# Kernel optimization log

Measured on AMD Instinct MI355X. Metric: run time of the kernel, lower is better.

The kernel has to match this reference:

```python
import jax, jax.numpy as jnp
import numpy as np

DIM = 192
NUM_HEADS = 6
KSZ = 7
MLP_RATIO = 4.0
LEVELS = 8
EPS = 1e-5


def layernorm(x, w, b):
    mu = jnp.mean(x, axis=-1, keepdims=True)
    var = jnp.mean(jnp.square(x - mu), axis=-1, keepdims=True)
    return (x - mu) * jax.lax.rsqrt(var + EPS) * w + b


def na2d(x, qkv_w, qkv_b, proj_w, proj_b, rpb):
    # Neighborhood attention 2D with relative position bias (NATTEN semantics:
    # window of KSZ x KSZ keys per query, clamped to stay inside the image).
    B, H, W, C = x.shape
    nh, hd = NUM_HEADS, C // NUM_HEADS
    scale = hd ** -0.5
    qkv = (x @ qkv_w.T + qkv_b).reshape(B, H, W, 3, nh, hd)
    q = qkv[..., 0, :, :] * scale  # [B,H,W,nh,hd]
    k = qkv[..., 1, :, :]
    v = qkv[..., 2, :, :]

    si = jnp.clip(jnp.arange(H) - KSZ // 2, 0, H - KSZ)
    idx_i = si[:, None] + jnp.arange(KSZ)  # [H,KSZ] row indices of each window
    sj = jnp.clip(jnp.arange(W) - KSZ // 2, 0, W - KSZ)
    idx_j = sj[:, None] + jnp.arange(KSZ)  # [W,KSZ]

    def gather_win(t):  # [B,H,W,nh,hd] -> [B,H,KSZ,W,KSZ,nh,hd]
        t = jnp.take(t, idx_i.reshape(-1), axis=1).reshape(B, H, KSZ, W, nh, hd)
        t = jnp.take(t, idx_j.reshape(-1), axis=3).reshape(B, H, KSZ, W, KSZ, nh, hd)
        return t

    kw = gather_win(k)
    vw = gather_win(v)

    # scores over the KSZ x KSZ neighborhood
    scores = jnp.einsum('bxynd,bxiyjnd->bxynij', q, kw)  # [B,H,W,nh,KSZ,KSZ]

    # relative position bias: rpb is [nh, 2K-1, 2K-1]
    rel_i = idx_i - jnp.arange(H)[:, None] + (KSZ - 1)  # [H,KSZ] in [0,2K-2]
    rel_j = idx_j - jnp.arange(W)[:, None] + (KSZ - 1)  # [W,KSZ]
    bias = rpb[:, rel_i][:, :, :, rel_j]  # [nh,H,KSZ,W,KSZ]
    scores = scores + bias.transpose(1, 3, 0, 2, 4)[None]

    attn = jax.nn.softmax(scores.reshape(B, H, W, nh, KSZ * KSZ), axis=-1)
    attn = attn.reshape(B, H, W, nh, KSZ, KSZ)
    out = jnp.einsum('bxynij,bxiyjnd->bxynd', attn, vw).reshape(B, H, W, C)
    return out @ proj_w.T + proj_b


def setup_inputs() -> dict:
    key = jax.random.key(0)
    ks = jax.random.split(key, 8)
    C = DIM
    hidden = int(C * MLP_RATIO)
    init = lambda k, shape: (jax.random.normal(k, shape, dtype=jnp.float32) * 0.02)
    return {
        'x': jax.random.normal(ks[0], (1, 128, 128, C), dtype=jnp.float32),
        'qkv_w': init(ks[1], (3 * C, C)),
        'qkv_b': jnp.zeros((3 * C,), jnp.float32),
        'proj_w': init(ks[2], (C, C)),
        'proj_b': jnp.zeros((C,), jnp.float32),
        'rpb': init(ks[3], (NUM_HEADS, 2 * KSZ - 1, 2 * KSZ - 1)),
        'ln1_w': jnp.ones((C,), jnp.float32),
        'ln1_b': jnp.zeros((C,), jnp.float32),
        'ln2_w': jnp.ones((C,), jnp.float32),
        'ln2_b': jnp.zeros((C,), jnp.float32),
        'fc1_w': init(ks[4], (hidden, C)),
        'fc1_b': jnp.zeros((hidden,), jnp.float32),
        'fc2_w': init(ks[5], (C, hidden)),
        'fc2_b': jnp.zeros((C,), jnp.float32),
        'gamma1': jnp.ones((LEVELS, C), jnp.float32),
        'gamma2': jnp.ones((LEVELS, C), jnp.float32),
        'quality': 4,
    }


def reference(x, qkv_w, qkv_b, proj_w, proj_b, rpb, ln1_w, ln1_b, ln2_w, ln2_b,
              fc1_w, fc1_b, fc2_w, fc2_b, gamma1, gamma2, quality):
    # eval-mode quality gating; quality is an integer so l = quality % 1 == 0
    s = int(quality) - 1
    g1 = jnp.abs(gamma1[s])
    g2 = jnp.abs(gamma2[s])

    shortcut = x
    h = layernorm(x, ln1_w, ln1_b)
    a = na2d(h, qkv_w, qkv_b, proj_w, proj_b, rpb)
    x = shortcut + g1 * a
    h2 = layernorm(x, ln2_w, ln2_b)
    m = jax.nn.gelu(h2 @ fc1_w.T + fc1_b, approximate=False) @ fc2_w.T + fc2_b
    x = x + g2 * m
    return x
```

## Files before the change

kernel.cpp:

```cpp
#include <hip/hip_runtime.h>
#include <hip/hip_bf16.h>
#include <math.h>

#define DIM 192
#define NHD 6
#define HD 32
#define KSZ 7
#define HID 768
#define IMH 128
#define IMW 128
#define NPIX (IMH*IMW)
#define WIN 14
#define KPAD 40

typedef __attribute__((ext_vector_type(8))) short short8;
typedef __attribute__((ext_vector_type(4))) float f32x4;

__global__ __launch_bounds__(256) void cvt_ln1(
    const float* __restrict__ qw, const float* __restrict__ pw,
    const float* __restrict__ f1, const float* __restrict__ f2,
    __hip_bfloat16* dq, __hip_bfloat16* dp, __hip_bfloat16* df1, __hip_bfloat16* df2,
    const float* __restrict__ x, const float* __restrict__ w, const float* __restrict__ b,
    __hip_bfloat16* __restrict__ hout)
{
    int blk = blockIdx.x, t = threadIdx.x;
    if (blk < 1728) {
        const float* s; __hip_bfloat16* d; int idx;
        if (blk < 432)       { s = qw; d = dq;  idx = blk * 256 + t; }
        else if (blk < 576)  { s = pw; d = dp;  idx = (blk - 432) * 256 + t; }
        else if (blk < 1152) { s = f1; d = df1; idx = (blk - 576) * 256 + t; }
        else                 { s = f2; d = df2; idx = (blk - 1152) * 256 + t; }
        d[idx] = __float2bfloat16(s[idx]);
        return;
    }
    int wid  = ((blk - 1728) * 256 + t) >> 6;
    int lane = t & 63;
    const float* xp = x + (size_t)wid * DIM;
    float v0 = xp[lane], v1 = xp[lane + 64], v2 = xp[lane + 128];
    float s = v0 + v1 + v2;
    #pragma unroll
    for (int off = 32; off > 0; off >>= 1) s += __shfl_down(s, off);
    float mu = __shfl(s, 0) * (1.0f / DIM);
    float d0 = v0 - mu, d1 = v1 - mu, d2 = v2 - mu;
    float q = d0*d0 + d1*d1 + d2*d2;
    #pragma unroll
    for (int off = 32; off > 0; off >>= 1) q += __shfl_down(q, off);
    float rstd = rsqrtf(__shfl(q, 0) * (1.0f / DIM) + 1e-5f);
    __hip_bfloat16* op = hout + (size_t)wid * DIM;
    op[lane]       = __float2bfloat16(d0 * rstd * w[lane]       + b[lane]);
    op[lane + 64]  = __float2bfloat16(d1 * rstd * w[lane + 64]  + b[lane + 64]);
    op[lane + 128] = __float2bfloat16(d2 * rstd * w[lane + 128] + b[lane + 128]);
}

__device__ __forceinline__ void gl_lds16(const void* g, void* l) {
    __builtin_amdgcn_global_load_lds(
        (const __attribute__((address_space(1))) void*)g,
        (__attribute__((address_space(3))) void*)l, 16, 0, 0);
}

template<int mode>
__global__ __launch_bounds__(256) void gemm_k192(
    const __hip_bfloat16* __restrict__ A, const __hip_bfloat16* __restrict__ W,
    const float* __restrict__ bias,
    float* outf, __hip_bfloat16* outb, __hip_bfloat16* kb, __hip_bfloat16* vb, int N)
{
    __shared__ __hip_bfloat16 As[128 * 192];
    __shared__ __hip_bfloat16 Bs[64 * 192];
    int tid = threadIdx.x;
    int wave = tid >> 6, lane = tid & 63;
    int m0 = blockIdx.x * 128, n0 = blockIdx.y * 64;
    int q = lane >> 4, col = lane & 15;
    int wm = (wave >> 1) * 64, wn = (wave & 1) * 32;

    const __hip_bfloat16* Ab = A + (size_t)m0 * 192;
    #pragma unroll
    for (int i = 0; i < 12; i++) {
        int c = i * 256 + tid;
        int r = c / 24, kc = c - r * 24;
        int g = kc ^ (r & 7);
        gl_lds16(Ab + r * 192 + g * 8, (char*)As + (i * 256 + wave * 64) * 16);
    }
    const __hip_bfloat16* Wb = W + (size_t)n0 * 192;
    #pragma unroll
    for (int i = 0; i < 6; i++) {
        int c = i * 256 + tid;
        int r = c / 24, kc = c - r * 24;
        int g = kc ^ (r & 7);
        gl_lds16(Wb + r * 192 + g * 8, (char*)Bs + (i * 256 + wave * 64) * 16);
    }
    __syncthreads();

    f32x4 acc[4][2] = {};
    #pragma unroll
    for (int ks = 0; ks < 6; ks++) {
        short8 af[4], bf[2];
        #pragma unroll
        for (int mi = 0; mi < 4; mi++) {
            int r = wm + mi * 16 + col;
            af[mi] = *(const short8*)&As[r * 192 + (((ks * 4 + q) ^ (r & 7)) * 8)];
        }
        #pragma unroll
        for (int ni = 0; ni < 2; ni++) {
            int r = wn + ni * 16 + col;
            bf[ni] = *(const short8*)&Bs[r * 192 + (((ks * 4 + q) ^ (r & 7)) * 8)];
        }
        #pragma unroll
        for (int mi = 0; mi < 4; mi++)
            #pragma unroll
            for (int ni = 0; ni < 2; ni++)
                acc[mi][ni] = __builtin_amdgcn_mfma_f32_16x16x32_bf16(
                    af[mi], bf[ni], acc[mi][ni], 0, 0, 0);
    }

    #pragma unroll
    for (int mi = 0; mi < 4; mi++) {
        #pragma unroll
        for (int r = 0; r < 4; r++) {
            int m = m0 + wm + mi * 16 + q * 4 + r;
            #pragma unroll
            for (int ni = 0; ni < 2; ni++) {
                int n = n0 + wn + ni * 16 + col;
                float v = acc[mi][ni][r] + bias[n];
                if (mode == 0) {
                    int h18 = n >> 5;
                    int sel = h18 / 6;
                    int head = h18 - sel * 6;
                    size_t idx = ((size_t)head * NPIX + m) * 32 + (n & 31);
                    if (sel == 0)      outf[idx] = v * 0.17677669529663687f;
                    else if (sel == 1) kb[idx] = __float2bfloat16(v);
                    else               vb[idx] = __float2bfloat16(v);
                } else {
                    float u = 0.7978845608f * (v + 0.044715f * v * v * v);
                    float t = 1.f - 2.f / (__expf(2.f * u) + 1.f);
                    v = 0.5f * v * (1.f + t);
                    outb[(size_t)m * N + n] = __float2bfloat16(v);
                }
            }
        }
    }
}

__global__ __launch_bounds__(256) void proj_ln(
    const __hip_bfloat16* __restrict__ A, const __hip_bfloat16* __restrict__ W,
    const float* __restrict__ bias,
    float* outf, __hip_bfloat16* hb, const float* __restrict__ resid,
    const float* __restrict__ gamma, const int* __restrict__ quality,
    const float* __restrict__ lnw, const float* __restrict__ lnb)
{
    __shared__ __hip_bfloat16 As[64 * 192];
    __shared__ __hip_bfloat16 Bs[192 * 192];
    int tid = threadIdx.x;
    int wave = tid >> 6, lane = tid & 63;
    int q = lane >> 4, col = lane & 15;
    int m0 = blockIdx.x * 64;

    const __hip_bfloat16* Ab = A + (size_t)m0 * 192;
    #pragma unroll
    for (int i = 0; i < 6; i++) {
        int c = i * 256 + tid;
        int r = c / 24, kc = c - r * 24;
        int g = kc ^ (r & 7);
        gl_lds16(Ab + r * 192 + g * 8, (char*)As + (i * 256 + wave * 64) * 16);
    }
    #pragma unroll
    for (int i = 0; i < 18; i++) {
        int c = i * 256 + tid;
        int r = c / 24, kc = c - r * 24;
        int g = kc ^ (r & 7);
        gl_lds16(W + r * 192 + g * 8, (char*)Bs + (i * 256 + wave * 64) * 16);
    }
    __syncthreads();

    f32x4 acc[12] = {};
    #pragma unroll
    for (int ks = 0; ks < 6; ks++) {
        int rA = wave * 16 + col;
        short8 af = *(const short8*)&As[rA * 192 + (((ks * 4 + q) ^ (rA & 7)) * 8)];
        #pragma unroll
        for (int f = 0; f < 12; f++) {
            int rB = f * 16 + col;
            short8 bf = *(const short8*)&Bs[rB * 192 + (((ks * 4 + q) ^ (rB & 7)) * 8)];
            acc[f] = __builtin_amdgcn_mfma_f32_16x16x32_bf16(af, bf, acc[f], 0, 0, 0);
        }
    }

    int s = quality[0] - 1;
    float v[12][4];
    #pragma unroll
    for (int f = 0; f < 12; f++) {
        int n = f * 16 + col;
        float bi = bias[n];
        float g = fabsf(gamma[s * DIM + n]);
        #pragma unroll
        for (int r = 0; r < 4; r++) {
            int m = m0 + wave * 16 + q * 4 + r;
            v[f][r] = resid[(size_t)m * DIM + n] + g * (acc[f][r] + bi);
            outf[(size_t)m * DIM + n] = v[f][r];
        }
    }
    float sm[4] = {}, sq[4] = {};
    #pragma unroll
    for (int f = 0; f < 12; f++)
        #pragma unroll
        for (int r = 0; r < 4; r++) { sm[r] += v[f][r]; sq[r] += v[f][r] * v[f][r]; }
    #pragma unroll
    for (int off = 1; off <= 8; off <<= 1) {
        #pragma unroll
        for (int r = 0; r < 4; r++) {
            sm[r] += __shfl_xor(sm[r], off);
            sq[r] += __shfl_xor(sq[r], off);
        }
    }
    float mu[4], rstd[4];
    #pragma unroll
    for (int r = 0; r < 4; r++) {
        mu[r] = sm[r] * (1.0f / DIM);
        float var = sq[r] * (1.0f / DIM) - mu[r] * mu[r];
        rstd[r] = rsqrtf(var + 1e-5f);
    }
    #pragma unroll
    for (int f = 0; f < 12; f++) {
        int n = f * 16 + col;
        float lw = lnw[n], lb = lnb[n];
        #pragma unroll
        for (int r = 0; r < 4; r++) {
            int m = m0 + wave * 16 + q * 4 + r;
            hb[(size_t)m * DIM + n] = __float2bfloat16((v[f][r] - mu[r]) * rstd[r] * lw + lb);
        }
    }
}

__global__ __launch_bounds__(512, 2) void mlp_fused(
    const __hip_bfloat16* __restrict__ A, const __hip_bfloat16* __restrict__ W1,
    const float* __restrict__ b1, const __hip_bfloat16* __restrict__ W2,
    const float* __restrict__ b2, float* __restrict__ outf,
    const float* __restrict__ gamma, const int* __restrict__ quality)
{
    __shared__ __hip_bfloat16 Ms[64 * 768];
    __shared__ __hip_bfloat16 Ws[2][64 * 192];
    int tid = threadIdx.x;
    int wave = tid >> 6, lane = tid & 63;
    int q = lane >> 4, col = lane & 15;
    int m0 = blockIdx.x * 64;
    int wm = (wave >> 1) * 16;
    int wh = (wave & 1);

    short8 af[6];
    {
        const __hip_bfloat16* ap = A + (size_t)(m0 + wm + col) * DIM;
        #pragma unroll
        for (int ks = 0; ks < 6; ks++)
            af[ks] = *(const short8*)(ap + ks * 32 + q * 8);
    }

    auto stage1 = [&](int t, int buf) {
        #pragma unroll
        for (int i = 0; i < 3; i++) {
            int c = i * 512 + tid;
            int r = c / 24, kc = c - r * 24;
            int g = kc ^ (r & 7);
            gl_lds16(W1 + (size_t)(t * 64 + r) * DIM + g * 8,
                     (char*)&Ws[buf][0] + (i * 512 + wave * 64) * 16);
        }
    };
    auto stage2 = [&](int ch, int buf) {
        #pragma unroll
        for (int i = 0; i < 3; i++) {
            int idx = i * 512 + tid;
            int r = idx >> 3, o = idx & 7;
            gl_lds16(W2 + (size_t)r * HID + ch * 64 + ((o ^ (r & 7)) * 8),
                     (char*)&Ws[buf][0] + (i * 512 + wave * 64) * 16);
        }
    };

    stage1(0, 0);
    for (int t = 0; t < 12; t++) {
        if (t < 11) stage1(t + 1, (t + 1) & 1);
        else        stage2(0, 0);
        asm volatile("s_waitcnt vmcnt(3)" ::: "memory");
        __builtin_amdgcn_s_barrier();
        const __hip_bfloat16* wsb = &Ws[t & 1][0];
        f32x4 acc[2] = {};
        #pragma unroll
        for (int ks = 0; ks < 6; ks++) {
            #pragma unroll
            for (int ni = 0; ni < 2; ni++) {
                int r = wh * 32 + ni * 16 + col;
                short8 bf = *(const short8*)&wsb[r * 192 + (((ks * 4 + q) ^ (r & 7)) * 8)];
                acc[ni] = __builtin_amdgcn_mfma_f32_16x16x32_bf16(af[ks], bf, acc[ni], 0, 0, 0);
            }
        }
        #pragma unroll
        for (int ni = 0; ni < 2; ni++) {
            int n = t * 64 + wh * 32 + ni * 16 + col;
            float bi = b1[n];
            int oct = n >> 3;
            #pragma unroll
            for (int r4 = 0; r4 < 4; r4++) {
                int row = wm + q * 4 + r4;
                float v = acc[ni][r4] + bi;
                float u = 0.7978845608f * (v + 0.044715f * v * v * v);
                float tt = 1.f - 2.f / (__expf(2.f * u) + 1.f);
                v = 0.5f * v * (1.f + tt);
                int osw = (oct & ~7) | ((oct ^ row) & 7);
                *(__hip_bfloat16*)((char*)Ms + row * 1536 + osw * 16 + (n & 7) * 2) =
                    __float2bfloat16(v);
            }
        }
        __builtin_amdgcn_s_barrier();
    }
    __syncthreads();

    int wn2 = wh * 96;
    f32x4 acc2[6] = {};
    for (int ch = 0; ch < 12; ch++) {
        stage2(ch < 11 ? ch + 1 : 11, (ch + 1) & 1);
        asm volatile("s_waitcnt vmcnt(3)" ::: "memory");
        __builtin_amdgcn_s_barrier();
        const __hip_bfloat16* wsb = &Ws[ch & 1][0];
        #pragma unroll
        for (int ks = 0; ks < 2; ks++) {
            int row = wm + col;
            int og = ch * 8 + ks * 4 + q;
            int osw = (og & ~7) | ((og ^ row) & 7);
            short8 a2 = *(const short8*)((char*)Ms + row * 1536 + osw * 16);
            #pragma unroll
            for (int f = 0; f < 6; f++) {
                int r = wn2 + f * 16 + col;
                short8 bf = *(const short8*)&wsb[r * 64 + (((ks * 4 + q) ^ (r & 7)) * 8)];
                acc2[f] = __builtin_amdgcn_mfma_f32_16x16x32_bf16(a2, bf, acc2[f], 0, 0, 0);
            }
        }
        __builtin_amdgcn_s_barrier();
    }
    int s = quality[0] - 1;
    #pragma unroll
    for (int f = 0; f < 6; f++) {
        int n = wn2 + f * 16 + col;
        float g = fabsf(gamma[s * DIM + n]);
        float bi = b2[n];
        #pragma unroll
        for (int r4 = 0; r4 < 4; r4++) {
            int m = m0 + wm + q * 4 + r4;
            outf[(size_t)m * DIM + n] = outf[(size_t)m * DIM + n] + g * (acc2[f][r4] + bi);
        }
    }
}

__device__ __forceinline__ void unpack8(const __hip_bfloat16* ptr, float* f) {
    short8 s8 = *(const short8*)ptr;
    union { short8 v; unsigned u[4]; } c; c.v = s8;
    #pragma unroll
    for (int w = 0; w < 4; w++) {
        f[2*w]   = __uint_as_float(c.u[w] << 16);
        f[2*w+1] = __uint_as_float(c.u[w] & 0xffff0000u);
    }
}

__global__ __launch_bounds__(256, 4) void attn_kernel3(
    const float* __restrict__ qbuf, const __hip_bfloat16* __restrict__ kbuf,
    const __hip_bfloat16* __restrict__ vbuf, const float* __restrict__ rpb,
    __hip_bfloat16* __restrict__ out)
{
    __shared__ __hip_bfloat16 Ks[WIN * WIN * KPAD];
    __shared__ __hip_bfloat16 Vs[WIN * WIN * KPAD];
    __shared__ float rpbs[169];

    int head = blockIdx.y;
    int tile = blockIdx.x;
    int ti0 = (tile >> 4) * 8;
    int tj0 = (tile & 15) * 8;
    int wi0 = ti0 - 3; wi0 = wi0 < 0 ? 0 : (wi0 > IMH - WIN ? IMH - WIN : wi0);
    int wj0 = tj0 - 3; wj0 = wj0 < 0 ? 0 : (wj0 > IMW - WIN ? IMW - WIN : wj0);

    int tid = threadIdx.x;
    const size_t hbase = (size_t)head * NPIX;

    for (int c = tid; c < 784; c += 256) {
        int i = c / 56, part = c - i * 56;
        int n = i * WIN + (part >> 2);
        int dp = part & 3;
        size_t goff = (hbase + (size_t)(wi0 + i) * IMW + wj0) * 32 + part * 8;
        short8 kk = *(const short8*)(kbuf + goff);
        short8 vv = *(const short8*)(vbuf + goff);
        *(short8*)&Ks[n * KPAD + dp * 8] = kk;
        *(short8*)&Vs[n * KPAD + dp * 8] = vv;
    }
    if (tid < 169) rpbs[tid] = rpb[head * 169 + tid];

    int p   = tid >> 2;
    int sub = tid & 3;
    int pi = ti0 + (p >> 3), pj = tj0 + (p & 7);
    int si = pi - 3; si = si < 0 ? 0 : (si > IMH - KSZ ? IMH - KSZ : si);
    int sj = pj - 3; sj = sj < 0 ? 0 : (sj > IMW - KSZ ? IMW - KSZ : sj);
    int bi = si - wi0, bj = sj - wj0;

    const float4* qp = (const float4*)(qbuf + (hbase + (size_t)(pi * IMW + pj)) * 32 + sub * 8);
    float4 q0 = qp[0], q1 = qp[1];
    float q[8] = {q0.x, q0.y, q0.z, q0.w, q1.x, q1.y, q1.z, q1.w};

    __syncthreads();

    float m = -1e30f, l = 0.f;
    float acc[8] = {};
    #pragma unroll
    for (int ki = 0; ki < KSZ; ki++) {
        int rbase = (bi + ki) * WIN + bj;
        const float* rb = &rpbs[(si + ki - pi + 6) * 13 + (sj - pj + 6)];
        float s7[KSZ];
        #pragma unroll
        for (int kj = 0; kj < KSZ; kj++) {
            float kf[8];
            unpack8(&Ks[(rbase + kj) * KPAD + sub * 8], kf);
            float d = q[0]*kf[0] + q[1]*kf[1] + q[2]*kf[2] + q[3]*kf[3]
                    + q[4]*kf[4] + q[5]*kf[5] + q[6]*kf[6] + q[7]*kf[7];
            d += __shfl_xor(d, 1);
            d += __shfl_xor(d, 2);
            s7[kj] = d + rb[kj];
        }
        float rmax = s7[0];
        #pragma unroll
        for (int kj = 1; kj < KSZ; kj++) rmax = fmaxf(rmax, s7[kj]);
        float mn = fmaxf(m, rmax);
        float co = __expf(m - mn);
        l *= co;
        #pragma unroll
        for (int e = 0; e < 8; e++) acc[e] *= co;
        #pragma unroll
        for (int kj = 0; kj < KSZ; kj++) {
            float pw = __expf(s7[kj] - mn);
            l += pw;
            float vf[8];
            unpack8(&Vs[(rbase + kj) * KPAD + sub * 8], vf);
            #pragma unroll
            for (int e = 0; e < 8; e++) acc[e] += pw * vf[e];
        }
        m = mn;
    }
    float rl = 1.f / l;
    __hip_bfloat16* op = out + (size_t)(pi * IMW + pj) * DIM + head * HD + sub * 8;
    #pragma unroll
    for (int e = 0; e < 8; e++) op[e] = __float2bfloat16(acc[e] * rl);
}

extern "C" void kernel_launch(void* const* d_in, const int* in_sizes, int n_in,
                              void* d_out, int out_size, void* d_ws, size_t ws_size,
                              hipStream_t stream)
{
    const float* x      = (const float*)d_in[0];
    const float* qkv_w  = (const float*)d_in[1];
    const float* qkv_b  = (const float*)d_in[2];
    const float* proj_w = (const float*)d_in[3];
    const float* proj_b = (const float*)d_in[4];
    const float* rpb    = (const float*)d_in[5];
    const float* ln1_w  = (const float*)d_in[6];
    const float* ln1_b  = (const float*)d_in[7];
    const float* ln2_w  = (const float*)d_in[8];
    const float* ln2_b  = (const float*)d_in[9];
    const float* fc1_w  = (const float*)d_in[10];
    const float* fc1_b  = (const float*)d_in[11];
    const float* fc2_w  = (const float*)d_in[12];
    const float* fc2_b  = (const float*)d_in[13];
    const float* gamma1 = (const float*)d_in[14];
    const float* gamma2 = (const float*)d_in[15];
    const int*   quality= (const int*)d_in[16];
    float* out = (float*)d_out;

    char* ws = (char*)d_ws;
    float*          qbuf   = (float*)ws;
    __hip_bfloat16* kbuf   = (__hip_bfloat16*)(ws + 12582912);
    __hip_bfloat16* vbuf   = (__hip_bfloat16*)(ws + 18874368);
    __hip_bfloat16* h      = (__hip_bfloat16*)(ws + 37748736);
    __hip_bfloat16* attn_b = (__hip_bfloat16*)(ws + 44040192);
    __hip_bfloat16* wq     = (__hip_bfloat16*)(ws + 50331648);
    __hip_bfloat16* wp     = (__hip_bfloat16*)(ws + 50552832);
    __hip_bfloat16* wf1    = (__hip_bfloat16*)(ws + 50626560);
    __hip_bfloat16* wf2    = (__hip_bfloat16*)(ws + 50921472);

    cvt_ln1<<<1728 + NPIX / 4, 256, 0, stream>>>(
        qkv_w, proj_w, fc1_w, fc2_w, wq, wp, wf1, wf2, x, ln1_w, ln1_b, h);
    gemm_k192<0><<<dim3(NPIX / 128, 9), 256, 0, stream>>>(
        h, wq, qkv_b, qbuf, nullptr, kbuf, vbuf, 576);
    attn_kernel3<<<dim3(256, NHD), 256, 0, stream>>>(qbuf, kbuf, vbuf, rpb, attn_b);
    proj_ln<<<NPIX / 64, 256, 0, stream>>>(
        attn_b, wp, proj_b, out, h, x, gamma1, quality, ln2_w, ln2_b);
    mlp_fused<<<256, 512, 0, stream>>>(
        h, wf1, fc1_b, wf2, fc2_b, out, gamma2, quality);
}
```

Measured before the change: 186.1 us.

## Fuse projection, LayerNorm2 and MLP into one tail kernel; vectorize weight conversion

Result: faster. 175.9 us (-5.5%).

```diff
diff --git a/kernel.cpp b/kernel.cpp
--- a/kernel.cpp
+++ b/kernel.cpp
@@ -24,16 +24,21 @@
     __hip_bfloat16* __restrict__ hout)
 {
     int blk = blockIdx.x, t = threadIdx.x;
-    if (blk < 1728) {
-        const float* s; __hip_bfloat16* d; int idx;
-        if (blk < 432)       { s = qw; d = dq;  idx = blk * 256 + t; }
-        else if (blk < 576)  { s = pw; d = dp;  idx = (blk - 432) * 256 + t; }
-        else if (blk < 1152) { s = f1; d = df1; idx = (blk - 576) * 256 + t; }
-        else                 { s = f2; d = df2; idx = (blk - 1152) * 256 + t; }
-        d[idx] = __float2bfloat16(s[idx]);
+    if (blk < 432) {
+        const float* s; __hip_bfloat16* d; int base;
+        if (blk < 108)      { s = qw; d = dq;  base = blk * 1024; }
+        else if (blk < 144) { s = pw; d = dp;  base = (blk - 108) * 1024; }
+        else if (blk < 288) { s = f1; d = df1; base = (blk - 144) * 1024; }
+        else                { s = f2; d = df2; base = (blk - 288) * 1024; }
+        int idx = base + t * 4;
+        float4 v4 = *(const float4*)(s + idx);
+        union { ushort4 u; __hip_bfloat16 h[4]; } o;
+        o.h[0] = __float2bfloat16(v4.x); o.h[1] = __float2bfloat16(v4.y);
+        o.h[2] = __float2bfloat16(v4.z); o.h[3] = __float2bfloat16(v4.w);
+        *(ushort4*)&d[idx] = o.u;
         return;
     }
-    int wid  = ((blk - 1728) * 256 + t) >> 6;
+    int wid  = ((blk - 432) * 256 + t) >> 6;
     int lane = t & 63;
     const float* xp = x + (size_t)wid * DIM;
     float v0 = xp[lane], v1 = xp[lane + 64], v2 = xp[lane + 128];
@@ -58,11 +63,10 @@
         (__attribute__((address_space(3))) void*)l, 16, 0, 0);
 }
 
-template<int mode>
-__global__ __launch_bounds__(256) void gemm_k192(
+__global__ __launch_bounds__(256) void qkv_gemm(
     const __hip_bfloat16* __restrict__ A, const __hip_bfloat16* __restrict__ W,
     const float* __restrict__ bias,
-    float* outf, __hip_bfloat16* outb, __hip_bfloat16* kb, __hip_bfloat16* vb, int N)
+    float* __restrict__ qb, __hip_bfloat16* __restrict__ kb, __hip_bfloat16* __restrict__ vb)
 {
     __shared__ __hip_bfloat16 As[128 * 192];
     __shared__ __hip_bfloat16 Bs[64 * 192];
@@ -121,146 +125,135 @@
             for (int ni = 0; ni < 2; ni++) {
                 int n = n0 + wn + ni * 16 + col;
                 float v = acc[mi][ni][r] + bias[n];
-                if (mode == 0) {
-                    int h18 = n >> 5;
-                    int sel = h18 / 6;
-                    int head = h18 - sel * 6;
-                    size_t idx = ((size_t)head * NPIX + m) * 32 + (n & 31);
-                    if (sel == 0)      outf[idx] = v * 0.17677669529663687f;
-                    else if (sel == 1) kb[idx] = __float2bfloat16(v);
-                    else               vb[idx] = __float2bfloat16(v);
-                } else {
-                    float u = 0.7978845608f * (v + 0.044715f * v * v * v);
-                    float t = 1.f - 2.f / (__expf(2.f * u) + 1.f);
-                    v = 0.5f * v * (1.f + t);
-                    outb[(size_t)m * N + n] = __float2bfloat16(v);
-                }
+                int h18 = n >> 5;
+                int sel = h18 / 6;
+                int head = h18 - sel * 6;
+                size_t idx = ((size_t)head * NPIX + m) * 32 + (n & 31);
+                if (sel == 0)      qb[idx] = v * 0.17677669529663687f;
+                else if (sel == 1) kb[idx] = __float2bfloat16(v);
+                else               vb[idx] = __float2bfloat16(v);
             }
         }
     }
 }
 
-__global__ __launch_bounds__(256) void proj_ln(
-    const __hip_bfloat16* __restrict__ A, const __hip_bfloat16* __restrict__ W,
-    const float* __restrict__ bias,
-    float* outf, __hip_bfloat16* hb, const float* __restrict__ resid,
-    const float* __restrict__ gamma, const int* __restrict__ quality,
-    const float* __restrict__ lnw, const float* __restrict__ lnb)
+__global__ __launch_bounds__(512, 2) void tail_fused(
+    const __hip_bfloat16* __restrict__ A, const __hip_bfloat16* __restrict__ Wp,
+    const float* __restrict__ pb, const float* __restrict__ resid,
+    const float* __restrict__ gamma1, const float* __restrict__ ln2w, const float* __restrict__ ln2b,
+    const __hip_bfloat16* __restrict__ W1, const float* __restrict__ b1,
+    const __hip_bfloat16* __restrict__ W2, const float* __restrict__ b2,
+    const float* __restrict__ gamma2, const int* __restrict__ quality,
+    float* __restrict__ outf)
 {
-    __shared__ __hip_bfloat16 As[64 * 192];
-    __shared__ __hip_bfloat16 Bs[192 * 192];
+    __shared__ __hip_bfloat16 arena[64 * 768];
+    __shared__ __hip_bfloat16 Wsb[2][64 * 192];
+    __shared__ float lnred[2][64][2];
+    __hip_bfloat16* Bsp = arena;
+    __hip_bfloat16* Hs  = arena + 192 * 192;
+
     int tid = threadIdx.x;
     int wave = tid >> 6, lane = tid & 63;
     int q = lane >> 4, col = lane & 15;
+    int wm = (wave >> 1) * 16, wh = wave & 1;
     int m0 = blockIdx.x * 64;
 
-    const __hip_bfloat16* Ab = A + (size_t)m0 * 192;
-    #pragma unroll
-    for (int i = 0; i < 6; i++) {
-        int c = i * 256 + tid;
+    const __hip_bfloat16* Ab = A + (size_t)m0 * DIM;
+    #pragma unroll
+    for (int i = 0; i < 3; i++) {
+        int c = i * 512 + tid;
         int r = c / 24, kc = c - r * 24;
-        int g = kc ^ (r & 7);
-        gl_lds16(Ab + r * 192 + g * 8, (char*)As + (i * 256 + wave * 64) * 16);
-    }
-    #pragma unroll
-    for (int i = 0; i < 18; i++) {
-        int c = i * 256 + tid;
+        gl_lds16(Ab + r * DIM + (kc ^ (r & 7)) * 8, (char*)Hs + (i * 512 + wave * 64) * 16);
+    }
+    #pragma unroll
+    for (int i = 0; i < 9; i++) {
+        int c = i * 512 + tid;
         int r = c / 24, kc = c - r * 24;
-        int g = kc ^ (r & 7);
-        gl_lds16(W + r * 192 + g * 8, (char*)Bs + (i * 256 + wave * 64) * 16);
-    }
-    __syncthreads();
-
-    f32x4 acc[12] = {};
+        gl_lds16(Wp + (size_t)r * DIM + (kc ^ (r & 7)) * 8, (char*)Bsp + (i * 512 + wave * 64) * 16);
+    }
+    __syncthreads();
+
+    f32x4 acc[6] = {};
     #pragma unroll
     for (int ks = 0; ks < 6; ks++) {
-        int rA = wave * 16 + col;
-        short8 af = *(const short8*)&As[rA * 192 + (((ks * 4 + q) ^ (rA & 7)) * 8)];
-        #pragma unroll
-        for (int f = 0; f < 12; f++) {
-            int rB = f * 16 + col;
-            short8 bf = *(const short8*)&Bs[rB * 192 + (((ks * 4 + q) ^ (rB & 7)) * 8)];
+        int rA = wm + col;
+        short8 af = *(const short8*)&Hs[rA * DIM + (((ks * 4 + q) ^ (rA & 7)) * 8)];
+        #pragma unroll
+        for (int f = 0; f < 6; f++) {
+            int rB = wh * 96 + f * 16 + col;
+            short8 bf = *(const short8*)&Bsp[rB * DIM + (((ks * 4 + q) ^ (rB & 7)) * 8)];
             acc[f] = __builtin_amdgcn_mfma_f32_16x16x32_bf16(af, bf, acc[f], 0, 0, 0);
         }
     }
 
     int s = quality[0] - 1;
-    float v[12][4];
-    #pragma unroll
-    for (int f = 0; f < 12; f++) {
-        int n = f * 16 + col;
-        float bi = bias[n];
-        float g = fabsf(gamma[s * DIM + n]);
+    float v[6][4];
+    float sm[4] = {}, sq[4] = {};
+    #pragma unroll
+    for (int f = 0; f < 6; f++) {
+        int n = wh * 96 + f * 16 + col;
+        float bi = pb[n];
+        float g = fabsf(gamma1[s * DIM + n]);
         #pragma unroll
         for (int r = 0; r < 4; r++) {
-            int m = m0 + wave * 16 + q * 4 + r;
+            int m = m0 + wm + q * 4 + r;
             v[f][r] = resid[(size_t)m * DIM + n] + g * (acc[f][r] + bi);
-            outf[(size_t)m * DIM + n] = v[f][r];
-        }
-    }
-    float sm[4] = {}, sq[4] = {};
-    #pragma unroll
-    for (int f = 0; f < 12; f++)
-        #pragma unroll
-        for (int r = 0; r < 4; r++) { sm[r] += v[f][r]; sq[r] += v[f][r] * v[f][r]; }
-    #pragma unroll
-    for (int off = 1; off <= 8; off <<= 1) {
+            sm[r] += v[f][r]; sq[r] += v[f][r] * v[f][r];
+        }
+    }
+    #pragma unroll
+    for (int off = 1; off <= 8; off <<= 1)
         #pragma unroll
         for (int r = 0; r < 4; r++) {
             sm[r] += __shfl_xor(sm[r], off);
             sq[r] += __shfl_xor(sq[r], off);
         }
-    }
+    if (col == 0) {
+        #pragma unroll
+        for (int r = 0; r < 4; r++) {
+            lnred[wh][wm + q * 4 + r][0] = sm[r];
+            lnred[wh][wm + q * 4 + r][1] = sq[r];
+        }
+    }
+    __syncthreads();
     float mu[4], rstd[4];
     #pragma unroll
     for (int r = 0; r < 4; r++) {
-        mu[r] = sm[r] * (1.0f / DIM);
-        float var = sq[r] * (1.0f / DIM) - mu[r] * mu[r];
+        int ml = wm + q * 4 + r;
+        float smt = lnred[0][ml][0] + lnred[1][ml][0];
+        float sqt = lnred[0][ml][1] + lnred[1][ml][1];
+        mu[r] = smt * (1.0f / DIM);
+        float var = sqt * (1.0f / DIM) - mu[r] * mu[r];
         rstd[r] = rsqrtf(var + 1e-5f);
     }
     #pragma unroll
-    for (int f = 0; f < 12; f++) {
-        int n = f * 16 + col;
-        float lw = lnw[n], lb = lnb[n];
+    for (int f = 0; f < 6; f++) {
+        int n = wh * 96 + f * 16 + col;
+        float lw = ln2w[n], lb = ln2b[n];
         #pragma unroll
         for (int r = 0; r < 4; r++) {
-            int m = m0 + wave * 16 + q * 4 + r;
-            hb[(size_t)m * DIM + n] = __float2bfloat16((v[f][r] - mu[r]) * rstd[r] * lw + lb);
-        }
-    }
-}
-
-__global__ __launch_bounds__(512, 2) void mlp_fused(
-    const __hip_bfloat16* __restrict__ A, const __hip_bfloat16* __restrict__ W1,
-    const float* __restrict__ b1, const __hip_bfloat16* __restrict__ W2,
-    const float* __restrict__ b2, float* __restrict__ outf,
-    const float* __restrict__ gamma, const int* __restrict__ quality)
-{
-    __shared__ __hip_bfloat16 Ms[64 * 768];
-    __shared__ __hip_bfloat16 Ws[2][64 * 192];
-    int tid = threadIdx.x;
-    int wave = tid >> 6, lane = tid & 63;
-    int q = lane >> 4, col = lane & 15;
-    int m0 = blockIdx.x * 64;
-    int wm = (wave >> 1) * 16;
-    int wh = (wave & 1);
-
-    short8 af[6];
+            int ml = wm + q * 4 + r;
+            Hs[ml * DIM + (((n >> 3) ^ (ml & 7)) * 8) + (n & 7)] =
+                __float2bfloat16((v[f][r] - mu[r]) * rstd[r] * lw + lb);
+        }
+    }
+    __syncthreads();
+    short8 af1[6];
     {
-        const __hip_bfloat16* ap = A + (size_t)(m0 + wm + col) * DIM;
+        int rowA = wm + col;
         #pragma unroll
         for (int ks = 0; ks < 6; ks++)
-            af[ks] = *(const short8*)(ap + ks * 32 + q * 8);
-    }
+            af1[ks] = *(const short8*)&Hs[rowA * DIM + (((ks * 4 + q) ^ (rowA & 7)) * 8)];
+    }
+    __syncthreads();
 
     auto stage1 = [&](int t, int buf) {
         #pragma unroll
         for (int i = 0; i < 3; i++) {
             int c = i * 512 + tid;
             int r = c / 24, kc = c - r * 24;
-            int g = kc ^ (r & 7);
-            gl_lds16(W1 + (size_t)(t * 64 + r) * DIM + g * 8,
-                     (char*)&Ws[buf][0] + (i * 512 + wave * 64) * 16);
+            gl_lds16(W1 + (size_t)(t * 64 + r) * DIM + (kc ^ (r & 7)) * 8,
+                     (char*)&Wsb[buf][0] + (i * 512 + wave * 64) * 16);
         }
     };
     auto stage2 = [&](int ch, int buf) {
@@ -269,9 +262,10 @@
             int idx = i * 512 + tid;
             int r = idx >> 3, o = idx & 7;
             gl_lds16(W2 + (size_t)r * HID + ch * 64 + ((o ^ (r & 7)) * 8),
-                     (char*)&Ws[buf][0] + (i * 512 + wave * 64) * 16);
+                     (char*)&Wsb[buf][0] + (i * 512 + wave * 64) * 16);
         }
     };
+    __hip_bfloat16* Ms = arena;
 
     stage1(0, 0);
     for (int t = 0; t < 12; t++) {
@@ -279,15 +273,15 @@
         else        stage2(0, 0);
         asm volatile("s_waitcnt vmcnt(3)" ::: "memory");
         __builtin_amdgcn_s_barrier();
-        const __hip_bfloat16* wsb = &Ws[t & 1][0];
-        f32x4 acc[2] = {};
+        const __hip_bfloat16* wsb = &Wsb[t & 1][0];
+        f32x4 a1[2] = {};
         #pragma unroll
         for (int ks = 0; ks < 6; ks++) {
             #pragma unroll
             for (int ni = 0; ni < 2; ni++) {
                 int r = wh * 32 + ni * 16 + col;
-                short8 bf = *(const short8*)&wsb[r * 192 + (((ks * 4 + q) ^ (r & 7)) * 8)];
-                acc[ni] = __builtin_amdgcn_mfma_f32_16x16x32_bf16(af[ks], bf, acc[ni], 0, 0, 0);
+                short8 bf = *(const short8*)&wsb[r * DIM + (((ks * 4 + q) ^ (r & 7)) * 8)];
+                a1[ni] = __builtin_amdgcn_mfma_f32_16x16x32_bf16(af1[ks], bf, a1[ni], 0, 0, 0);
             }
         }
         #pragma unroll
@@ -298,13 +292,13 @@
             #pragma unroll
             for (int r4 = 0; r4 < 4; r4++) {
                 int row = wm + q * 4 + r4;
-                float v = acc[ni][r4] + bi;
-                float u = 0.7978845608f * (v + 0.044715f * v * v * v);
+                float vv = a1[ni][r4] + bi;
+                float u = 0.7978845608f * (vv + 0.044715f * vv * vv * vv);
                 float tt = 1.f - 2.f / (__expf(2.f * u) + 1.f);
-                v = 0.5f * v * (1.f + tt);
+                vv = 0.5f * vv * (1.f + tt);
                 int osw = (oct & ~7) | ((oct ^ row) & 7);
                 *(__hip_bfloat16*)((char*)Ms + row * 1536 + osw * 16 + (n & 7) * 2) =
-                    __float2bfloat16(v);
+                    __float2bfloat16(vv);
             }
         }
         __builtin_amdgcn_s_barrier();
@@ -317,7 +311,7 @@
         stage2(ch < 11 ? ch + 1 : 11, (ch + 1) & 1);
         asm volatile("s_waitcnt vmcnt(3)" ::: "memory");
         __builtin_amdgcn_s_barrier();
-        const __hip_bfloat16* wsb = &Ws[ch & 1][0];
+        const __hip_bfloat16* wsb = &Wsb[ch & 1][0];
         #pragma unroll
         for (int ks = 0; ks < 2; ks++) {
             int row = wm + col;
@@ -333,16 +327,15 @@
         }
         __builtin_amdgcn_s_barrier();
     }
-    int s = quality[0] - 1;
     #pragma unroll
     for (int f = 0; f < 6; f++) {
         int n = wn2 + f * 16 + col;
-        float g = fabsf(gamma[s * DIM + n]);
+        float g = fabsf(gamma2[s * DIM + n]);
         float bi = b2[n];
         #pragma unroll
         for (int r4 = 0; r4 < 4; r4++) {
             int m = m0 + wm + q * 4 + r4;
-            outf[(size_t)m * DIM + n] = outf[(size_t)m * DIM + n] + g * (acc2[f][r4] + bi);
+            outf[(size_t)m * DIM + n] = v[f][r4] + g * (acc2[f][r4] + bi);
         }
     }
 }
@@ -477,13 +470,12 @@
     __hip_bfloat16* wf1    = (__hip_bfloat16*)(ws + 50626560);
     __hip_bfloat16* wf2    = (__hip_bfloat16*)(ws + 50921472);
 
-    cvt_ln1<<<1728 + NPIX / 4, 256, 0, stream>>>(
+    cvt_ln1<<<432 + NPIX / 4, 256, 0, stream>>>(
         qkv_w, proj_w, fc1_w, fc2_w, wq, wp, wf1, wf2, x, ln1_w, ln1_b, h);
-    gemm_k192<0><<<dim3(NPIX / 128, 9), 256, 0, stream>>>(
-        h, wq, qkv_b, qbuf, nullptr, kbuf, vbuf, 576);
+    qkv_gemm<<<dim3(NPIX / 128, 9), 256, 0, stream>>>(
+        h, wq, qkv_b, qbuf, kbuf, vbuf);
     attn_kernel3<<<dim3(256, NHD), 256, 0, stream>>>(qbuf, kbuf, vbuf, rpb, attn_b);
-    proj_ln<<<NPIX / 64, 256, 0, stream>>>(
-        attn_b, wp, proj_b, out, h, x, gamma1, quality, ln2_w, ln2_b);
-    mlp_fused<<<256, 512, 0, stream>>>(
-        h, wf1, fc1_b, wf2, fc2_b, out, gamma2, quality);
-}
+    tail_fused<<<256, 512, 0, stream>>>(
+        attn_b, wp, proj_b, x, gamma1, ln2_w, ln2_b,
+        wf1, fc1_b, wf2, fc2_b, gamma2, quality, out);
+}
```
